# Kernel optimization log

Hardware: AMD Instinct MI355X
Metric: run time of the kernel (lower is better)

Reference implementation:

```python
import jax, jax.numpy as jnp
import numpy as np

LEAKY_SLOPE = 0.01  # PyTorch F.leaky_relu default


def setup_inputs() -> dict:
    key = jax.random.key(0)
    ks = jax.random.split(key, 6)
    N, E, IN, OUT = 100000, 1000000, 256, 64
    x = jax.random.normal(ks[0], (N, IN), dtype=jnp.float32)
    edge_index = jax.random.randint(ks[1], (2, E), 0, N, dtype=jnp.int64)
    edge_weight = jax.random.uniform(ks[2], (E,), dtype=jnp.float32)
    W_lin = jax.random.normal(ks[3], (IN, OUT), dtype=jnp.float32) / np.sqrt(IN)
    b_lin = jax.random.normal(ks[4], (OUT,), dtype=jnp.float32) * 0.01
    W_att = jax.random.normal(ks[5], (2 * OUT, 1), dtype=jnp.float32) / np.sqrt(2 * OUT)
    b_att = jnp.zeros((1,), dtype=jnp.float32)
    return {"x": x, "edge_index": edge_index, "edge_weight": edge_weight,
            "W_lin": W_lin, "b_lin": b_lin, "W_att": W_att, "b_att": b_att}


def reference(x, edge_index, edge_weight, W_lin, b_lin, W_att, b_att):
    # h = Linear(x): [N, OUT]
    h = x @ W_lin + b_lin
    row, col = edge_index[0], edge_index[1]
    OUT = h.shape[-1]
    # attention(cat([h_i, h_j])) == h_i @ W_att[:OUT] + h_j @ W_att[OUT:] + b_att.
    # Project per-node first (N x OUT GEMV) then gather scalars per edge — same math,
    # avoids materializing the [E, 2*OUT] concatenation.
    a_src = (h @ W_att[:OUT]).squeeze(-1)   # [N]
    a_dst = (h @ W_att[OUT:]).squeeze(-1)   # [N]
    scores = a_src[row] + a_dst[col] + b_att[0]          # [E]
    scores = jax.nn.leaky_relu(scores, LEAKY_SLOPE)
    # Global softmax over all edges (dim=0 in the original on an [E,1] tensor)
    scores = jax.nn.softmax(scores, axis=0)
    scores = scores * edge_weight                        # [E]
    msgs = scores[:, None] * h[col]                      # [E, OUT]
    agg = jnp.zeros_like(h).at[row].add(msgs)            # scatter-add to [N, OUT]
    return jax.nn.relu(h + agg)
```

## Files before the change

kernel.cpp:

```cpp
#include <hip/hip_runtime.h>

#define LEAKY 0.01f
#define CAP 15

typedef __attribute__((ext_vector_type(8))) short short8;
typedef __attribute__((ext_vector_type(4))) float f32x4;

__device__ __forceinline__ unsigned short f2bf(float f) {
    unsigned u = __float_as_uint(f);
    return (unsigned short)((u + 0x7FFFu + ((u >> 16) & 1u)) >> 16);
}
__device__ __forceinline__ float bf2f(unsigned short u) {
    return __uint_as_float((unsigned)u << 16);
}

__global__ __launch_bounds__(256) void k_prep(
    const float* __restrict__ W, unsigned short* __restrict__ wt,
    float* __restrict__ gsum)
{
    int t = blockIdx.x * 256 + threadIdx.x;
    if (t == 0) *gsum = 0.f;
    int n = t >> 8;
    int k = t & 255;
    unsigned short bf = f2bf(W[k * 64 + n]);
    int slot = (k >> 3) ^ (n & 7);
    wt[(n * 512 + slot * 16 + (k & 7) * 2) >> 1] = bf;
}

__global__ __launch_bounds__(256, 4) void k_linear(
    const float* __restrict__ x, const unsigned short* __restrict__ wt_g,
    const float* __restrict__ bl, const float* __restrict__ Wa,
    unsigned short* __restrict__ hb, float* __restrict__ a_src,
    float* __restrict__ a_dst, unsigned* __restrict__ ell, int N)
{
    __shared__ __align__(16) char wtlds[32768];
    int t = threadIdx.x;
    int r0 = blockIdx.x * 64;

    #pragma unroll
    for (int i = 0; i < 8; ++i) {
        int f8 = t + i * 256;
        ((uint4*)wtlds)[f8] = ((const uint4*)wt_g)[f8];
    }
    __syncthreads();

    int lane = t & 63;
    int w = t >> 6;
    int cl = lane & 15;
    int lg = lane >> 4;

    int arow = w * 16 + cl;
    int grow = r0 + arow;
    const float* xrow = x + (size_t)min(grow, N - 1) * 256;

    short8 a[8];
    #pragma unroll
    for (int kk = 0; kk < 8; ++kk) {
        int k0 = (kk * 4 + lg) * 8;
        float4 v0 = *(const float4*)(xrow + k0);
        float4 v1 = *(const float4*)(xrow + k0 + 4);
        short8 av;
        av[0] = (short)f2bf(v0.x); av[1] = (short)f2bf(v0.y);
        av[2] = (short)f2bf(v0.z); av[3] = (short)f2bf(v0.w);
        av[4] = (short)f2bf(v1.x); av[5] = (short)f2bf(v1.y);
        av[6] = (short)f2bf(v1.z); av[7] = (short)f2bf(v1.w);
        a[kk] = av;
    }

    f32x4 acc[4];
    #pragma unroll
    for (int n = 0; n < 4; ++n) acc[n] = (f32x4){0.f, 0.f, 0.f, 0.f};

    #pragma unroll
    for (int n = 0; n < 4; ++n) {
        int brow = n * 16 + cl;
        #pragma unroll
        for (int kk = 0; kk < 8; ++kk) {
            int ak = kk * 4 + lg;
            short8 bfr = *(const short8*)(wtlds + brow * 512 + ((ak ^ (brow & 7)) << 4));
            acc[n] = __builtin_amdgcn_mfma_f32_16x16x32_bf16(a[kk], bfr, acc[n], 0, 0, 0);
        }
    }

    float asj[4] = {0.f, 0.f, 0.f, 0.f}, adj[4] = {0.f, 0.f, 0.f, 0.f};
    #pragma unroll
    for (int n = 0; n < 4; ++n) {
        int col = n * 16 + cl;
        float bias = bl[col];
        float wa1 = Wa[col], wa2 = Wa[64 + col];
        #pragma unroll
        for (int j = 0; j < 4; ++j) {
            float hv = acc[n][j] + bias;
            int gr = r0 + w * 16 + lg * 4 + j;
            if (gr < N) hb[(size_t)gr * 64 + col] = f2bf(hv);
            asj[j] = fmaf(hv, wa1, asj[j]);
            adj[j] = fmaf(hv, wa2, adj[j]);
        }
    }
    #pragma unroll
    for (int off = 1; off < 16; off <<= 1) {
        #pragma unroll
        for (int j = 0; j < 4; ++j) {
            asj[j] += __shfl_xor(asj[j], off);
            adj[j] += __shfl_xor(adj[j], off);
        }
    }
    if (cl == 0) {
        #pragma unroll
        for (int j = 0; j < 4; ++j) {
            int gr = r0 + w * 16 + lg * 4 + j;
            if (gr < N) {
                a_src[gr] = asj[j];
                a_dst[gr] = adj[j];
                ell[(size_t)gr * 16] = 0u;
            }
        }
    }
}

__global__ __launch_bounds__(256) void k_bucket(
    const int* __restrict__ ei, const float* __restrict__ ew,
    const float* __restrict__ a_src, const float* __restrict__ a_dst,
    const float* __restrict__ batt, unsigned* __restrict__ ell,
    float* __restrict__ gsum, int E)
{
    int e0 = (blockIdx.x * 256 + threadIdx.x) * 4;
    float psum = 0.f;
    if (e0 + 3 < E) {
        int4 rr = *(const int4*)(ei + e0);
        int4 cc = *(const int4*)(ei + E + e0);
        float4 wv = *(const float4*)(ew + e0);
        float b = batt[0];
        float s0 = a_src[rr.x] + a_dst[cc.x] + b;
        float s1 = a_src[rr.y] + a_dst[cc.y] + b;
        float s2 = a_src[rr.z] + a_dst[cc.z] + b;
        float s3 = a_src[rr.w] + a_dst[cc.w] + b;
        s0 = (s0 > 0.f) ? s0 : LEAKY * s0;
        s1 = (s1 > 0.f) ? s1 : LEAKY * s1;
        s2 = (s2 > 0.f) ? s2 : LEAKY * s2;
        s3 = (s3 > 0.f) ? s3 : LEAKY * s3;
        float p0 = __expf(s0), p1 = __expf(s1), p2 = __expf(s2), p3 = __expf(s3);
        unsigned* r0 = ell + (size_t)rr.x * 16;
        unsigned* r1 = ell + (size_t)rr.y * 16;
        unsigned* r2 = ell + (size_t)rr.z * 16;
        unsigned* r3 = ell + (size_t)rr.w * 16;
        unsigned k0 = atomicAdd(r0, 1u);
        unsigned k1 = atomicAdd(r1, 1u);
        unsigned k2 = atomicAdd(r2, 1u);
        unsigned k3 = atomicAdd(r3, 1u);
        if (k0 < CAP) r0[1 + k0] = ((unsigned)cc.x << 15) | ((__float_as_uint(p0 * wv.x) >> 16) & 0x7FFFu);
        if (k1 < CAP) r1[1 + k1] = ((unsigned)cc.y << 15) | ((__float_as_uint(p1 * wv.y) >> 16) & 0x7FFFu);
        if (k2 < CAP) r2[1 + k2] = ((unsigned)cc.z << 15) | ((__float_as_uint(p2 * wv.z) >> 16) & 0x7FFFu);
        if (k3 < CAP) r3[1 + k3] = ((unsigned)cc.w << 15) | ((__float_as_uint(p3 * wv.w) >> 16) & 0x7FFFu);
        psum = (p0 + p1) + (p2 + p3);
    } else {
        for (int e = e0; e < E; ++e) {
            int r = ei[e], c = ei[E + e];
            float s = a_src[r] + a_dst[c] + batt[0];
            s = (s > 0.f) ? s : LEAKY * s;
            float p = __expf(s);
            unsigned* rw = ell + (size_t)r * 16;
            unsigned k = atomicAdd(rw, 1u);
            if (k < CAP) rw[1 + k] =
                ((unsigned)c << 15) | ((__float_as_uint(p * ew[e]) >> 16) & 0x7FFFu);
            psum += p;
        }
    }
    #pragma unroll
    for (int off = 32; off; off >>= 1) psum += __shfl_xor(psum, off);
    __shared__ float wsum[4];
    int lane = threadIdx.x & 63, w = threadIdx.x >> 6;
    if (lane == 0) wsum[w] = psum;
    __syncthreads();
    if (threadIdx.x == 0) atomicAdd(gsum, wsum[0] + wsum[1] + wsum[2] + wsum[3]);
}

__global__ __launch_bounds__(256) void k_aggregate(
    const unsigned* __restrict__ ell, const unsigned short* __restrict__ hb,
    const float* __restrict__ gsum, float4* __restrict__ out4, int N)
{
    int r = blockIdx.x * 4 + (threadIdx.x >> 6);
    if (r >= N) return;
    int lane = threadIdx.x & 63;
    int sub = lane >> 4, l = lane & 15;
    const unsigned* row = ell + (size_t)r * 16;
    int d = min((int)row[0], CAP);
    float4 acc = make_float4(0.f, 0.f, 0.f, 0.f);
    for (int p = sub; p < d; p += 4) {
        unsigned rec = row[1 + p];
        float cf = __uint_as_float((rec & 0x7FFFu) << 16);
        int c = rec >> 15;
        ushort4 hv = *(const ushort4*)(hb + (size_t)c * 64 + l * 4);
        acc.x = fmaf(cf, bf2f(hv.x), acc.x);
        acc.y = fmaf(cf, bf2f(hv.y), acc.y);
        acc.z = fmaf(cf, bf2f(hv.z), acc.z);
        acc.w = fmaf(cf, bf2f(hv.w), acc.w);
    }
    acc.x += __shfl_xor(acc.x, 16); acc.y += __shfl_xor(acc.y, 16);
    acc.z += __shfl_xor(acc.z, 16); acc.w += __shfl_xor(acc.w, 16);
    acc.x += __shfl_xor(acc.x, 32); acc.y += __shfl_xor(acc.y, 32);
    acc.z += __shfl_xor(acc.z, 32); acc.w += __shfl_xor(acc.w, 32);
    if (sub == 0) {
        float inv = 1.0f / (*gsum);
        ushort4 hv = *(const ushort4*)(hb + (size_t)r * 64 + l * 4);
        float4 o;
        o.x = fmaxf(fmaf(inv, acc.x, bf2f(hv.x)), 0.f);
        o.y = fmaxf(fmaf(inv, acc.y, bf2f(hv.y)), 0.f);
        o.z = fmaxf(fmaf(inv, acc.z, bf2f(hv.z)), 0.f);
        o.w = fmaxf(fmaf(inv, acc.w, bf2f(hv.w)), 0.f);
        out4[(size_t)r * 16 + l] = o;
    }
}

extern "C" void kernel_launch(void* const* d_in, const int* in_sizes, int n_in,
                              void* d_out, int out_size, void* d_ws, size_t ws_size,
                              hipStream_t stream)
{
    const float* x    = (const float*)d_in[0];
    const int*   ei   = (const int*)d_in[1];
    const float* ew   = (const float*)d_in[2];
    const float* Wlin = (const float*)d_in[3];
    const float* blin = (const float*)d_in[4];
    const float* Watt = (const float*)d_in[5];
    const float* batt = (const float*)d_in[6];
    float* out = (float*)d_out;

    int N = in_sizes[0] / 256;
    int E = in_sizes[2];

    char* p = (char*)d_ws;
    unsigned short* hb = (unsigned short*)p; p += (size_t)N * 64 * 2;
    float* a_src    = (float*)p;  p += (size_t)N * 4;
    float* a_dst    = (float*)p;  p += (size_t)N * 4;
    unsigned short* wt = (unsigned short*)p; p += 65536;
    float* gsum     = (float*)p;  p += 64;
    unsigned* ell   = (unsigned*)p;

    k_prep<<<64, 256, 0, stream>>>(Wlin, wt, gsum);
    k_linear<<<(N + 63) / 64, 256, 0, stream>>>(x, wt, blin, Watt, hb,
                                                a_src, a_dst, ell, N);
    k_bucket<<<(E / 4 + 255) / 256, 256, 0, stream>>>(ei, ew, a_src, a_dst, batt,
                                                      ell, gsum, E);
    k_aggregate<<<(N + 3) / 4, 256, 0, stream>>>(ell, hb, gsum, (float4*)out, N);
}
```

Measured before the change: 132.7 us.

## Precompute attention projections via folded GEMV and overlap bucketing with linear GEMM

Folds the attention weights into the linear weights so a_src/a_dst are computed by a separate fp32 GEMV over x, breaking the dependency between the linear GEMM and edge bucketing. The linear GEMM and bucketing then run in one fused launch with blocks split by role, letting atomics-heavy bucketing overlap with MFMA work. The trade-off is reading x a second time and adding a kernel launch.

```diff
diff --git a/kernel.cpp b/kernel.cpp
--- a/kernel.cpp
+++ b/kernel.cpp
@@ -15,27 +15,147 @@
 }
 
 __global__ __launch_bounds__(256) void k_prep(
-    const float* __restrict__ W, unsigned short* __restrict__ wt,
-    float* __restrict__ gsum)
-{
-    int t = blockIdx.x * 256 + threadIdx.x;
-    if (t == 0) *gsum = 0.f;
-    int n = t >> 8;
-    int k = t & 255;
-    unsigned short bf = f2bf(W[k * 64 + n]);
-    int slot = (k >> 3) ^ (n & 7);
-    wt[(n * 512 + slot * 16 + (k & 7) * 2) >> 1] = bf;
-}
-
-__global__ __launch_bounds__(256, 4) void k_linear(
+    const float* __restrict__ W, const float* __restrict__ bl,
+    const float* __restrict__ Wa, unsigned short* __restrict__ wt,
+    float* __restrict__ wv, float* __restrict__ gsum)
+{
+    if (blockIdx.x < 64) {
+        int t = blockIdx.x * 256 + threadIdx.x;
+        int n = t >> 8;
+        int k = t & 255;
+        unsigned short bf = f2bf(W[k * 64 + n]);
+        int slot = (k >> 3) ^ (n & 7);
+        wt[(n * 512 + slot * 16 + (k & 7) * 2) >> 1] = bf;
+    } else {
+        int k = threadIdx.x;
+        float s1 = 0.f, s2 = 0.f;
+        const float* wr = W + k * 64;
+        #pragma unroll
+        for (int n = 0; n < 64; ++n) {
+            float wkn = wr[n];
+            s1 = fmaf(wkn, Wa[n], s1);
+            s2 = fmaf(wkn, Wa[64 + n], s2);
+        }
+        wv[k] = s1;
+        wv[256 + k] = s2;
+        if (k == 0) {
+            float c1 = 0.f, c2 = 0.f;
+            #pragma unroll
+            for (int n = 0; n < 64; ++n) {
+                c1 = fmaf(bl[n], Wa[n], c1);
+                c2 = fmaf(bl[n], Wa[64 + n], c2);
+            }
+            wv[512] = c1;
+            wv[513] = c2;
+            *gsum = 0.f;
+        }
+    }
+}
+
+__global__ __launch_bounds__(256) void k_gemv(
+    const float* __restrict__ x, const float* __restrict__ wv,
+    float* __restrict__ a_src, float* __restrict__ a_dst,
+    unsigned* __restrict__ ell, int N)
+{
+    int t = threadIdx.x;
+    int lane = t & 63;
+    int w = t >> 6;
+    int cl = lane & 15, lg = lane >> 4;
+    int grow = blockIdx.x * 64 + w * 16 + cl;
+    const float* xrow = x + (size_t)min(grow, N - 1) * 256;
+    float c1 = wv[512], c2 = wv[513];
+
+    float as = 0.f, ad = 0.f;
+    #pragma unroll
+    for (int kk = 0; kk < 8; ++kk) {
+        int k0 = (kk * 4 + lg) * 8;
+        float4 v0 = *(const float4*)(xrow + k0);
+        float4 v1 = *(const float4*)(xrow + k0 + 4);
+        float4 u0 = *(const float4*)(wv + k0);
+        float4 u1 = *(const float4*)(wv + k0 + 4);
+        float4 q0 = *(const float4*)(wv + 256 + k0);
+        float4 q1 = *(const float4*)(wv + 256 + k0 + 4);
+        as += v0.x*u0.x + v0.y*u0.y + v0.z*u0.z + v0.w*u0.w
+            + v1.x*u1.x + v1.y*u1.y + v1.z*u1.z + v1.w*u1.w;
+        ad += v0.x*q0.x + v0.y*q0.y + v0.z*q0.z + v0.w*q0.w
+            + v1.x*q1.x + v1.y*q1.y + v1.z*q1.z + v1.w*q1.w;
+    }
+    as += __shfl_xor(as, 16); ad += __shfl_xor(ad, 16);
+    as += __shfl_xor(as, 32); ad += __shfl_xor(ad, 32);
+    if (lg == 0 && grow < N) {
+        a_src[grow] = as + c1;
+        a_dst[grow] = ad + c2;
+        ell[(size_t)grow * 16] = 0u;
+    }
+}
+
+__global__ __launch_bounds__(256, 4) void k_fused(
     const float* __restrict__ x, const unsigned short* __restrict__ wt_g,
-    const float* __restrict__ bl, const float* __restrict__ Wa,
-    unsigned short* __restrict__ hb, float* __restrict__ a_src,
-    float* __restrict__ a_dst, unsigned* __restrict__ ell, int N)
-{
-    __shared__ __align__(16) char wtlds[32768];
+    const float* __restrict__ bl,
+    const int* __restrict__ ei, const float* __restrict__ ew,
+    const float* __restrict__ a_src, const float* __restrict__ a_dst,
+    const float* __restrict__ batt,
+    unsigned short* __restrict__ hb, unsigned* __restrict__ ell,
+    float* __restrict__ gsum, int N, int E, int nb_bucket)
+{
+    __shared__ __align__(16) char lds[32768];
     int t = threadIdx.x;
-    int r0 = blockIdx.x * 64;
+
+    if ((int)blockIdx.x < nb_bucket) {
+        int e0 = (blockIdx.x * 256 + t) * 4;
+        float psum = 0.f;
+        if (e0 + 3 < E) {
+            int4 rr = *(const int4*)(ei + e0);
+            int4 cc = *(const int4*)(ei + E + e0);
+            float4 wvv = *(const float4*)(ew + e0);
+            float b = batt[0];
+            float s0 = a_src[rr.x] + a_dst[cc.x] + b;
+            float s1 = a_src[rr.y] + a_dst[cc.y] + b;
+            float s2 = a_src[rr.z] + a_dst[cc.z] + b;
+            float s3 = a_src[rr.w] + a_dst[cc.w] + b;
+            s0 = (s0 > 0.f) ? s0 : LEAKY * s0;
+            s1 = (s1 > 0.f) ? s1 : LEAKY * s1;
+            s2 = (s2 > 0.f) ? s2 : LEAKY * s2;
+            s3 = (s3 > 0.f) ? s3 : LEAKY * s3;
+            float p0 = __expf(s0), p1 = __expf(s1), p2 = __expf(s2), p3 = __expf(s3);
+            unsigned* r0 = ell + (size_t)rr.x * 16;
+            unsigned* r1 = ell + (size_t)rr.y * 16;
+            unsigned* r2 = ell + (size_t)rr.z * 16;
+            unsigned* r3 = ell + (size_t)rr.w * 16;
+            unsigned k0 = atomicAdd(r0, 1u);
+            unsigned k1 = atomicAdd(r1, 1u);
+            unsigned k2 = atomicAdd(r2, 1u);
+            unsigned k3 = atomicAdd(r3, 1u);
+            if (k0 < CAP) r0[1 + k0] = ((unsigned)cc.x << 15) | ((__float_as_uint(p0 * wvv.x) >> 16) & 0x7FFFu);
+            if (k1 < CAP) r1[1 + k1] = ((unsigned)cc.y << 15) | ((__float_as_uint(p1 * wvv.y) >> 16) & 0x7FFFu);
+            if (k2 < CAP) r2[1 + k2] = ((unsigned)cc.z << 15) | ((__float_as_uint(p2 * wvv.z) >> 16) & 0x7FFFu);
+            if (k3 < CAP) r3[1 + k3] = ((unsigned)cc.w << 15) | ((__float_as_uint(p3 * wvv.w) >> 16) & 0x7FFFu);
+            psum = (p0 + p1) + (p2 + p3);
+        } else {
+            for (int e = e0; e < E; ++e) {
+                int r = ei[e], c = ei[E + e];
+                float s = a_src[r] + a_dst[c] + batt[0];
+                s = (s > 0.f) ? s : LEAKY * s;
+                float p = __expf(s);
+                unsigned* rw = ell + (size_t)r * 16;
+                unsigned k = atomicAdd(rw, 1u);
+                if (k < CAP) rw[1 + k] =
+                    ((unsigned)c << 15) | ((__float_as_uint(p * ew[e]) >> 16) & 0x7FFFu);
+                psum += p;
+            }
+        }
+        #pragma unroll
+        for (int off = 32; off; off >>= 1) psum += __shfl_xor(psum, off);
+        float* wsum = (float*)lds;
+        int lane = t & 63, w = t >> 6;
+        if (lane == 0) wsum[w] = psum;
+        __syncthreads();
+        if (t == 0) atomicAdd(gsum, wsum[0] + wsum[1] + wsum[2] + wsum[3]);
+        return;
+    }
+
+    char* wtlds = lds;
+    int r0 = ((int)blockIdx.x - nb_bucket) * 64;
 
     #pragma unroll
     for (int i = 0; i < 8; ++i) {
@@ -49,8 +169,7 @@
     int cl = lane & 15;
     int lg = lane >> 4;
 
-    int arow = w * 16 + cl;
-    int grow = r0 + arow;
+    int grow = r0 + w * 16 + cl;
     const float* xrow = x + (size_t)min(grow, N - 1) * 256;
 
     short8 a[8];
@@ -82,97 +201,16 @@
         }
     }
 
-    float asj[4] = {0.f, 0.f, 0.f, 0.f}, adj[4] = {0.f, 0.f, 0.f, 0.f};
     #pragma unroll
     for (int n = 0; n < 4; ++n) {
         int col = n * 16 + cl;
         float bias = bl[col];
-        float wa1 = Wa[col], wa2 = Wa[64 + col];
-        #pragma unroll
-        for (int j = 0; j < 4; ++j) {
-            float hv = acc[n][j] + bias;
-            int gr = r0 + w * 16 + lg * 4 + j;
-            if (gr < N) hb[(size_t)gr * 64 + col] = f2bf(hv);
-            asj[j] = fmaf(hv, wa1, asj[j]);
-            adj[j] = fmaf(hv, wa2, adj[j]);
-        }
-    }
-    #pragma unroll
-    for (int off = 1; off < 16; off <<= 1) {
-        #pragma unroll
-        for (int j = 0; j < 4; ++j) {
-            asj[j] += __shfl_xor(asj[j], off);
-            adj[j] += __shfl_xor(adj[j], off);
-        }
-    }
-    if (cl == 0) {
         #pragma unroll
         for (int j = 0; j < 4; ++j) {
             int gr = r0 + w * 16 + lg * 4 + j;
-            if (gr < N) {
-                a_src[gr] = asj[j];
-                a_dst[gr] = adj[j];
-                ell[(size_t)gr * 16] = 0u;
-            }
-        }
-    }
-}
-
-__global__ __launch_bounds__(256) void k_bucket(
-    const int* __restrict__ ei, const float* __restrict__ ew,
-    const float* __restrict__ a_src, const float* __restrict__ a_dst,
-    const float* __restrict__ batt, unsigned* __restrict__ ell,
-    float* __restrict__ gsum, int E)
-{
-    int e0 = (blockIdx.x * 256 + threadIdx.x) * 4;
-    float psum = 0.f;
-    if (e0 + 3 < E) {
-        int4 rr = *(const int4*)(ei + e0);
-        int4 cc = *(const int4*)(ei + E + e0);
-        float4 wv = *(const float4*)(ew + e0);
-        float b = batt[0];
-        float s0 = a_src[rr.x] + a_dst[cc.x] + b;
-        float s1 = a_src[rr.y] + a_dst[cc.y] + b;
-        float s2 = a_src[rr.z] + a_dst[cc.z] + b;
-        float s3 = a_src[rr.w] + a_dst[cc.w] + b;
-        s0 = (s0 > 0.f) ? s0 : LEAKY * s0;
-        s1 = (s1 > 0.f) ? s1 : LEAKY * s1;
-        s2 = (s2 > 0.f) ? s2 : LEAKY * s2;
-        s3 = (s3 > 0.f) ? s3 : LEAKY * s3;
-        float p0 = __expf(s0), p1 = __expf(s1), p2 = __expf(s2), p3 = __expf(s3);
-        unsigned* r0 = ell + (size_t)rr.x * 16;
-        unsigned* r1 = ell + (size_t)rr.y * 16;
-        unsigned* r2 = ell + (size_t)rr.z * 16;
-        unsigned* r3 = ell + (size_t)rr.w * 16;
-        unsigned k0 = atomicAdd(r0, 1u);
-        unsigned k1 = atomicAdd(r1, 1u);
-        unsigned k2 = atomicAdd(r2, 1u);
-        unsigned k3 = atomicAdd(r3, 1u);
-        if (k0 < CAP) r0[1 + k0] = ((unsigned)cc.x << 15) | ((__float_as_uint(p0 * wv.x) >> 16) & 0x7FFFu);
-        if (k1 < CAP) r1[1 + k1] = ((unsigned)cc.y << 15) | ((__float_as_uint(p1 * wv.y) >> 16) & 0x7FFFu);
-        if (k2 < CAP) r2[1 + k2] = ((unsigned)cc.z << 15) | ((__float_as_uint(p2 * wv.z) >> 16) & 0x7FFFu);
-        if (k3 < CAP) r3[1 + k3] = ((unsigned)cc.w << 15) | ((__float_as_uint(p3 * wv.w) >> 16) & 0x7FFFu);
-        psum = (p0 + p1) + (p2 + p3);
-    } else {
-        for (int e = e0; e < E; ++e) {
-            int r = ei[e], c = ei[E + e];
-            float s = a_src[r] + a_dst[c] + batt[0];
-            s = (s > 0.f) ? s : LEAKY * s;
-            float p = __expf(s);
-            unsigned* rw = ell + (size_t)r * 16;
-            unsigned k = atomicAdd(rw, 1u);
-            if (k < CAP) rw[1 + k] =
-                ((unsigned)c << 15) | ((__float_as_uint(p * ew[e]) >> 16) & 0x7FFFu);
-            psum += p;
-        }
-    }
-    #pragma unroll
-    for (int off = 32; off; off >>= 1) psum += __shfl_xor(psum, off);
-    __shared__ float wsum[4];
-    int lane = threadIdx.x & 63, w = threadIdx.x >> 6;
-    if (lane == 0) wsum[w] = psum;
-    __syncthreads();
-    if (threadIdx.x == 0) atomicAdd(gsum, wsum[0] + wsum[1] + wsum[2] + wsum[3]);
+            if (gr < N) hb[(size_t)gr * 64 + col] = f2bf(acc[n][j] + bias);
+        }
+    }
 }
 
 __global__ __launch_bounds__(256) void k_aggregate(
@@ -233,13 +271,17 @@
     float* a_src    = (float*)p;  p += (size_t)N * 4;
     float* a_dst    = (float*)p;  p += (size_t)N * 4;
     unsigned short* wt = (unsigned short*)p; p += 65536;
+    float* wv       = (float*)p;  p += 2560;
     float* gsum     = (float*)p;  p += 64;
     unsigned* ell   = (unsigned*)p;
 
-    k_prep<<<64, 256, 0, stream>>>(Wlin, wt, gsum);
-    k_linear<<<(N + 63) / 64, 256, 0, stream>>>(x, wt, blin, Watt, hb,
-                                                a_src, a_dst, ell, N);
-    k_bucket<<<(E / 4 + 255) / 256, 256, 0, stream>>>(ei, ew, a_src, a_dst, batt,
-                                                      ell, gsum, E);
+    int nb_bucket = (E / 4 + 255) / 256;
+    int nb_linear = (N + 63) / 64;
+
+    k_prep<<<65, 256, 0, stream>>>(Wlin, blin, Watt, wt, wv, gsum);
+    k_gemv<<<(N + 63) / 64, 256, 0, stream>>>(x, wv, a_src, a_dst, ell, N);
+    k_fused<<<nb_bucket + nb_linear, 256, 0, stream>>>(
+        x, wt, blin, ei, ew, a_src, a_dst, batt, hb, ell, gsum,
+        N, E, nb_bucket);
     k_aggregate<<<(N + 3) / 4, 256, 0, stream>>>(ell, hb, gsum, (float4*)out, N);
 }
```

Measured after the change: 148.0 us. 11.5% more time.
